# Kernel optimization log

Measured on AMD Instinct MI355X. Metric: run time of the kernel, lower is better.

## Reference

```python
import jax, jax.numpy as jnp
import numpy as np

VOCAB, EMB, RNN, OUT = 32000, 512, 1024, 4


def setup_inputs() -> dict:
    key = jax.random.key(0)
    ks = jax.random.split(key, 8)
    stdv = 1.0 / np.sqrt(RNN)
    u = lambda k, shape, s: jax.random.uniform(k, shape, jnp.float32, -s, s)
    return {
        "x": jax.random.randint(ks[0], (512, 64), 0, VOCAB),
        "emb_table": jax.random.normal(ks[1], (VOCAB, EMB), jnp.float32),
        "w_ih": u(ks[2], (3 * RNN, EMB), stdv),
        "w_hh": u(ks[3], (3 * RNN, RNN), stdv),
        "b_ih": u(ks[4], (3 * RNN,), stdv),
        "b_hh": u(ks[5], (3 * RNN,), stdv),
        "fc_w": u(ks[6], (OUT, RNN), 1.0 / np.sqrt(RNN)),
        "fc_b": u(ks[7], (OUT,), 1.0 / np.sqrt(RNN)),
    }


def reference(x, emb_table, w_ih, w_hh, b_ih, b_hh, fc_w, fc_b):
    # x: [T, B] int indices
    T, B = x.shape
    embedded = emb_table[x]  # [T, B, EMB]
    # precompute input projections for all timesteps at once: [T, B, 3*RNN]
    gi_all = jnp.einsum('tbe,ge->tbg', embedded, w_ih) + b_ih

    def step(h, gi):
        gh = h @ w_hh.T + b_hh  # [B, 3*RNN]
        i_r, i_i, i_n = jnp.split(gi, 3, axis=1)
        h_r, h_i, h_n = jnp.split(gh, 3, axis=1)
        r = jax.nn.sigmoid(i_r + h_r)
        z = jax.nn.sigmoid(i_i + h_i)
        n = jnp.tanh(i_n + r * h_n)
        hy = z * n + (1.0 - z) * h  # note: matches GRUCellExposed (z gates newgate)
        return hy, hy

    h0 = jnp.zeros((B, w_hh.shape[1]), embedded.dtype)
    h_last, _ = jax.lax.scan(step, h0, gi_all)
    out = h_last @ fc_w.T + fc_b  # [B, OUT]
    return out
```

## Files before the change

kernel.cpp:

```cpp
#include <hip/hip_runtime.h>
#include <hip/hip_bf16.h>

typedef __attribute__((ext_vector_type(8))) short  short8;
typedef __attribute__((ext_vector_type(4))) float  f32x4;

#define T_TOTAL 512
#define BATCH   64
#define VOCAB   32000
#define EMB     512
#define RNN     1024
#define G3      3072
#define WROWS   48
#define WPAD    1032
#define RPAD    18
#define NWG     256
#define NGRP    4
#define SMEM_BYTES (WROWS * WPAD * 2 + 4 * WROWS * RPAD * 4)

__device__ __forceinline__ unsigned short f2bf(float f) {
    union { float f; unsigned int u; } v; v.f = f;
    unsigned int r = v.u + 0x7fffu + ((v.u >> 16) & 1u);
    return (unsigned short)(r >> 16);
}
__device__ __forceinline__ float bf2f(unsigned short h) {
    union { unsigned int u; float f; } v; v.u = ((unsigned int)h) << 16;
    return v.f;
}
__device__ __forceinline__ float sigmoidf_(float x) { return 1.f / (1.f + __expf(-x)); }
__device__ __forceinline__ float tanhf_(float x) {
    float ax = fabsf(x);
    float e2 = __expf(-2.f * ax);
    float t  = (1.f - e2) / (1.f + e2);
    return x < 0.f ? -t : t;
}

__device__ __forceinline__ void gbar_arrive(unsigned int* flags, int sidx,
                                            unsigned int ph) {
    __syncthreads();
    if (threadIdx.x == 0)
        __hip_atomic_store(&flags[sidx], ph,
                           __ATOMIC_RELAXED, __HIP_MEMORY_SCOPE_AGENT);
}
__device__ __forceinline__ void gbar_wait(unsigned int* flags, unsigned int ph) {
    if (threadIdx.x < 64) {
        for (;;) {
            unsigned int v = __hip_atomic_load(&flags[threadIdx.x],
                                               __ATOMIC_RELAXED,
                                               __HIP_MEMORY_SCOPE_AGENT);
            if (__all(v >= ph)) break;
            __builtin_amdgcn_s_sleep(1);
        }
    }
    __syncthreads();
}

__global__ void bar_init(unsigned int* bar) {
    for (int i = threadIdx.x; i < NGRP * 256; i += 256) bar[i] = 0;
}

__global__ __launch_bounds__(256) void cvt_bf16_kernel(
    const float* __restrict__ s, unsigned short* __restrict__ d, int n8)
{
    const int i = blockIdx.x * 256 + threadIdx.x;
    if (i >= n8) return;
    const float4 a = ((const float4*)s)[i * 2];
    const float4 b = ((const float4*)s)[i * 2 + 1];
    short8 v;
    v[0] = f2bf(a.x); v[1] = f2bf(a.y); v[2] = f2bf(a.z); v[3] = f2bf(a.w);
    v[4] = f2bf(b.x); v[5] = f2bf(b.y); v[6] = f2bf(b.z); v[7] = f2bf(b.w);
    ((short8*)d)[i] = v;
}

template<bool BF>
__global__ __launch_bounds__(256) void gi_kernel(
    const int* __restrict__ x, const void* __restrict__ embp,
    const void* __restrict__ wihp, const float* __restrict__ b_ih,
    unsigned short* __restrict__ gi, int t0)
{
    __shared__ __align__(16) unsigned short Asm[128 * 40];
    __shared__ __align__(16) unsigned short Bsm[128 * 40];

    const int tid = threadIdx.x;
    const int m0 = blockIdx.x * 128;
    const int n0 = blockIdx.y * 128;

    const int r    = tid >> 1;
    const int half = tid & 1;
    const int xi = x[t0 * BATCH + m0 + r];
    unsigned short* adst = &Asm[r * 40 + half * 16];
    unsigned short* bdst = &Bsm[r * 40 + half * 16];

    const int lane = tid & 63, wv = tid >> 6;
    const int m_off = (wv & 1) * 64, n_off = (wv >> 1) * 64;
    const int lr = lane & 15, lq = lane >> 4;

    f32x4 acc[4][4];
    #pragma unroll
    for (int i = 0; i < 4; ++i)
        #pragma unroll
        for (int j = 0; j < 4; ++j) acc[i][j] = (f32x4){0.f, 0.f, 0.f, 0.f};

    if constexpr (BF) {
        const unsigned short* arow = (const unsigned short*)embp
                                   + (size_t)xi * EMB + half * 16;
        const unsigned short* brow = (const unsigned short*)wihp
                                   + (size_t)(n0 + r) * EMB + half * 16;
        for (int k0 = 0; k0 < EMB; k0 += 32) {
            const short8 av0 = *(const short8*)(arow + k0);
            const short8 av1 = *(const short8*)(arow + k0 + 8);
            const short8 bv0 = *(const short8*)(brow + k0);
            const short8 bv1 = *(const short8*)(brow + k0 + 8);
            __syncthreads();
            *(short8*)(adst)     = av0;
            *(short8*)(adst + 8) = av1;
            *(short8*)(bdst)     = bv0;
            *(short8*)(bdst + 8) = bv1;
            __syncthreads();

            short8 fa[4], fb[4];
            #pragma unroll
            for (int i = 0; i < 4; ++i) {
                fa[i] = *(const short8*)&Asm[(m_off + i * 16 + lr) * 40 + lq * 8];
                fb[i] = *(const short8*)&Bsm[(n_off + i * 16 + lr) * 40 + lq * 8];
            }
            #pragma unroll
            for (int mi = 0; mi < 4; ++mi)
                #pragma unroll
                for (int ni = 0; ni < 4; ++ni)
                    acc[mi][ni] = __builtin_amdgcn_mfma_f32_16x16x32_bf16(
                        fa[mi], fb[ni], acc[mi][ni], 0, 0, 0);
        }
    } else {
        const float* arow = (const float*)embp + (size_t)xi * EMB + half * 16;
        const float* brow = (const float*)wihp + (size_t)(n0 + r) * EMB + half * 16;
        for (int k0 = 0; k0 < EMB; k0 += 32) {
            const float4 a0 = *(const float4*)(arow + k0);
            const float4 a1 = *(const float4*)(arow + k0 + 4);
            const float4 a2 = *(const float4*)(arow + k0 + 8);
            const float4 a3 = *(const float4*)(arow + k0 + 12);
            const float4 b0 = *(const float4*)(brow + k0);
            const float4 b1 = *(const float4*)(brow + k0 + 4);
            const float4 b2 = *(const float4*)(brow + k0 + 8);
            const float4 b3 = *(const float4*)(brow + k0 + 12);
            __syncthreads();
            short8 av0, av1, bv0, bv1;
            av0[0]=f2bf(a0.x); av0[1]=f2bf(a0.y); av0[2]=f2bf(a0.z); av0[3]=f2bf(a0.w);
            av0[4]=f2bf(a1.x); av0[5]=f2bf(a1.y); av0[6]=f2bf(a1.z); av0[7]=f2bf(a1.w);
            av1[0]=f2bf(a2.x); av1[1]=f2bf(a2.y); av1[2]=f2bf(a2.z); av1[3]=f2bf(a2.w);
            av1[4]=f2bf(a3.x); av1[5]=f2bf(a3.y); av1[6]=f2bf(a3.z); av1[7]=f2bf(a3.w);
            bv0[0]=f2bf(b0.x); bv0[1]=f2bf(b0.y); bv0[2]=f2bf(b0.z); bv0[3]=f2bf(b0.w);
            bv0[4]=f2bf(b1.x); bv0[5]=f2bf(b1.y); bv0[6]=f2bf(b1.z); bv0[7]=f2bf(b1.w);
            bv1[0]=f2bf(b2.x); bv1[1]=f2bf(b2.y); bv1[2]=f2bf(b2.z); bv1[3]=f2bf(b2.w);
            bv1[4]=f2bf(b3.x); bv1[5]=f2bf(b3.y); bv1[6]=f2bf(b3.z); bv1[7]=f2bf(b3.w);
            *(short8*)(adst)     = av0;
            *(short8*)(adst + 8) = av1;
            *(short8*)(bdst)     = bv0;
            *(short8*)(bdst + 8) = bv1;
            __syncthreads();

            short8 fa[4], fb[4];
            #pragma unroll
            for (int i = 0; i < 4; ++i) {
                fa[i] = *(const short8*)&Asm[(m_off + i * 16 + lr) * 40 + lq * 8];
                fb[i] = *(const short8*)&Bsm[(n_off + i * 16 + lr) * 40 + lq * 8];
            }
            #pragma unroll
            for (int mi = 0; mi < 4; ++mi)
                #pragma unroll
                for (int ni = 0; ni < 4; ++ni)
                    acc[mi][ni] = __builtin_amdgcn_mfma_f32_16x16x32_bf16(
                        fa[mi], fb[ni], acc[mi][ni], 0, 0, 0);
        }
    }

    float bia[4];
    #pragma unroll
    for (int ni = 0; ni < 4; ++ni) bia[ni] = b_ih[n0 + n_off + ni * 16 + lr];
    #pragma unroll
    for (int mi = 0; mi < 4; ++mi)
        #pragma unroll
        for (int ni = 0; ni < 4; ++ni) {
            const int n = n0 + n_off + ni * 16 + lr;
            #pragma unroll
            for (int q = 0; q < 4; ++q) {
                const int m = m0 + m_off + mi * 16 + lq * 4 + q;
                gi[(size_t)m * G3 + n] = f2bf(acc[mi][ni][q] + bia[ni]);
            }
        }
}

__global__ __launch_bounds__(256, 1) void rec_kernel(
    const unsigned short* __restrict__ gi,
    const float* __restrict__ w_hh, const float* __restrict__ b_hh,
    unsigned short* __restrict__ hb0, unsigned short* __restrict__ hb1,
    float* __restrict__ hf, unsigned int* bar, int t0, int nsteps, int pbase)
{
    extern __shared__ __align__(16) char smem[];
    unsigned short* Wsm = (unsigned short*)smem;
    float (*red)[WROWS][RPAD] = (float (*)[WROWS][RPAD])(smem + WROWS * WPAD * 2);

    const int tid = threadIdx.x;
    const int wg  = blockIdx.x;
    const int grp = wg & 3, sidx = wg >> 2;
    const int b0 = grp * 16, j0 = sidx * 16;
    unsigned int* flags = &bar[grp * 64];

    #pragma unroll 4
    for (int it = 0; it < 48; ++it) {
        const int i   = it * 256 + tid;
        const int row = i >> 8;
        const int c4  = (i & 255) * 4;
        const int gate = row >> 4, uu = row & 15;
        const float4 v = *(const float4*)(w_hh + (size_t)(gate * RNN + j0 + uu) * RNN + c4);
        unsigned short* dst = &Wsm[row * WPAD + c4];
        dst[0] = f2bf(v.x); dst[1] = f2bf(v.y); dst[2] = f2bf(v.z); dst[3] = f2bf(v.w);
    }

    const int u  = tid & 15;
    const int bl = tid >> 4;
    const int j  = j0 + u;
    const int b  = b0 + bl;
    const float bhr = b_hh[j], bhi = b_hh[RNN + j], bhn = b_hh[2 * RNN + j];

    float h_reg;
    if (t0 == 0) {
        h_reg = 0.f;
        if ((u & 1) == 0)
            __hip_atomic_store((unsigned int*)&hb0[b * RNN + j], 0u,
                               __ATOMIC_RELAXED, __HIP_MEMORY_SCOPE_AGENT);
    } else {
        h_reg = hf[b * RNN + j];
    }
    gbar_arrive(flags, sidx, (unsigned)(pbase + 1));

    size_t gb = (size_t)b * G3 + j0 + u;
    float gir = bf2f(gi[gb]);
    float gii = bf2f(gi[gb + RNN]);
    float gin = bf2f(gi[gb + 2 * RNN]);
    gbar_wait(flags, (unsigned)(pbase + 1));

    const int lane = tid & 63, kq = tid >> 6;
    const int lr = lane & 15, lq = lane >> 4;
    const unsigned short* wbase = Wsm + kq * 256 + lq * 8;
    const size_t hoff = ((size_t)(b0 + lr) * RNN + kq * 256 + lq * 8) >> 2;

    for (int t = 0; t < nsteps; ++t) {
        const unsigned short* hrd = (t & 1) ? hb1 : hb0;
        unsigned short*       hwr = (t & 1) ? hb0 : hb1;

        union { unsigned long long q[2]; short8 s8; } hv[8];
        const unsigned long long* hp = (const unsigned long long*)hrd + hoff;
        #pragma unroll
        for (int ks = 0; ks < 8; ++ks) {
            hv[ks].q[0] = __hip_atomic_load(hp + ks * 8,     __ATOMIC_RELAXED,
                                            __HIP_MEMORY_SCOPE_AGENT);
            hv[ks].q[1] = __hip_atomic_load(hp + ks * 8 + 1, __ATOMIC_RELAXED,
                                            __HIP_MEMORY_SCOPE_AGENT);
        }

        f32x4 acc[3];
        acc[0] = (f32x4){0.f, 0.f, 0.f, 0.f};
        acc[1] = (f32x4){0.f, 0.f, 0.f, 0.f};
        acc[2] = (f32x4){0.f, 0.f, 0.f, 0.f};
        #pragma unroll
        for (int ks = 0; ks < 8; ++ks) {
            const int k = ks * 32;
            #pragma unroll
            for (int gt = 0; gt < 3; ++gt) {
                const short8 a = *(const short8*)(wbase + (gt * 16 + lr) * WPAD + k);
                acc[gt] = __builtin_amdgcn_mfma_f32_16x16x32_bf16(a, hv[ks].s8,
                                                                  acc[gt], 0, 0, 0);
            }
        }
        #pragma unroll
        for (int gt = 0; gt < 3; ++gt)
            #pragma unroll
            for (int q = 0; q < 4; ++q)
                red[kq][gt * 16 + lq * 4 + q][lr] = acc[gt][q];
        __syncthreads();

        const float ghr = red[0][u][bl]      + red[1][u][bl]
                        + red[2][u][bl]      + red[3][u][bl];
        const float ghi = red[0][16 + u][bl] + red[1][16 + u][bl]
                        + red[2][16 + u][bl] + red[3][16 + u][bl];
        const float ghn = red[0][32 + u][bl] + red[1][32 + u][bl]
                        + red[2][32 + u][bl] + red[3][32 + u][bl];
        const float rr = sigmoidf_(gir + ghr + bhr);
        const float zz = sigmoidf_(gii + ghi + bhi);
        const float nn = tanhf_(gin + rr * (ghn + bhn));
        h_reg = zz * nn + (1.f - zz) * h_reg;

        unsigned int hvv = (unsigned int)f2bf(h_reg);
        unsigned int ovv = __shfl_xor((int)hvv, 1);
        if ((u & 1) == 0)
            __hip_atomic_store((unsigned int*)&hwr[b * RNN + j],
                               hvv | (ovv << 16), __ATOMIC_RELAXED,
                               __HIP_MEMORY_SCOPE_AGENT);

        gbar_arrive(flags, sidx, (unsigned)(pbase + 2 + t));
        const int tn = (t + 1 < nsteps) ? t + 1 : t;
        gb = ((size_t)tn * BATCH + b) * G3 + j0 + u;
        const float ngr = bf2f(gi[gb]);
        const float ngi = bf2f(gi[gb + RNN]);
        const float ngn = bf2f(gi[gb + 2 * RNN]);
        gbar_wait(flags, (unsigned)(pbase + 2 + t));
        gir = ngr; gii = ngi; gin = ngn;
    }
    hf[b * RNN + j] = h_reg;
}

__global__ __launch_bounds__(256) void out_kernel(
    const float* __restrict__ hf, const float* __restrict__ fc_w,
    const float* __restrict__ fc_b, float* __restrict__ out)
{
    __shared__ float red[256];
    const int bidx = blockIdx.x, tid = threadIdx.x;
    const int o = tid & 3, seg = tid >> 2;
    const float* hp = hf   + (size_t)bidx * RNN + seg * 16;
    const float* wp = fc_w + (size_t)o * RNN + seg * 16;
    float acc = 0.f;
    #pragma unroll
    for (int i = 0; i < 16; ++i) acc += hp[i] * wp[i];
    red[tid] = acc;
    __syncthreads();
    if (tid < 4) {
        float sv = fc_b[tid];
        #pragma unroll 8
        for (int q = 0; q < 64; ++q) sv += red[q * 4 + tid];
        out[bidx * 4 + tid] = sv;
    }
}

extern "C" void kernel_launch(void* const* d_in, const int* in_sizes, int n_in,
                              void* d_out, int out_size, void* d_ws, size_t ws_size,
                              hipStream_t stream)
{
    const int*   x     = (const int*)d_in[0];
    const float* emb   = (const float*)d_in[1];
    const float* w_ih  = (const float*)d_in[2];
    const float* w_hh  = (const float*)d_in[3];
    const float* b_ih  = (const float*)d_in[4];
    const float* b_hh  = (const float*)d_in[5];
    const float* fc_w  = (const float*)d_in[6];
    const float* fc_b  = (const float*)d_in[7];
    float*       out   = (float*)d_out;

    const size_t bar_b   = (size_t)NGRP * 256 * 4;
    const size_t aux     = 2 * (size_t)BATCH * RNN * 2
                         + (size_t)BATCH * RNN * 4 + bar_b;
    const size_t gi_full = (size_t)T_TOTAL * BATCH * G3 * 2;
    const size_t embbf_b = (size_t)VOCAB * EMB * 2;
    const size_t wihbf_b = (size_t)G3 * EMB * 2;
    const bool fused  = ws_size >= gi_full + aux;
    const bool bfpath = ws_size >= gi_full + aux + embbf_b + wihbf_b;
    const int tch  = fused ? 512 : 128;
    const int nchk = T_TOTAL / tch;

    char* ws = (char*)d_ws;
    unsigned short* gi_buf = (unsigned short*)ws;
    size_t off = (size_t)tch * BATCH * G3 * 2;
    unsigned short* hb0 = (unsigned short*)(ws + off); off += (size_t)BATCH * RNN * 2;
    unsigned short* hb1 = (unsigned short*)(ws + off); off += (size_t)BATCH * RNN * 2;
    float*          hf  = (float*)(ws + off);          off += (size_t)BATCH * RNN * 4;
    unsigned int*   bar = (unsigned int*)(ws + off);   off += bar_b;
    unsigned short* embbf = (unsigned short*)(ws + off); off += embbf_b;
    unsigned short* wihbf = (unsigned short*)(ws + off);

    hipFuncSetAttribute((const void*)rec_kernel,
                        hipFuncAttributeMaxDynamicSharedMemorySize, SMEM_BYTES);

    bar_init<<<dim3(1), dim3(256), 0, stream>>>(bar);
    if (bfpath) {
        cvt_bf16_kernel<<<dim3((VOCAB * EMB / 8 + 255) / 256), dim3(256), 0, stream>>>(
            emb, embbf, VOCAB * EMB / 8);
        cvt_bf16_kernel<<<dim3((G3 * EMB / 8 + 255) / 256), dim3(256), 0, stream>>>(
            w_ih, wihbf, G3 * EMB / 8);
    }

    for (int c = 0; c < nchk; ++c) {
        int t0 = c * tch, ns = tch, pb = c * (tch + 1);
        if (bfpath)
            gi_kernel<true><<<dim3(tch * BATCH / 128, 24), dim3(256), 0, stream>>>(
                x, (const void*)embbf, (const void*)wihbf, b_ih, gi_buf, t0);
        else
            gi_kernel<false><<<dim3(tch * BATCH / 128, 24), dim3(256), 0, stream>>>(
                x, (const void*)emb, (const void*)w_ih, b_ih, gi_buf, t0);
        void* args[10];
        args[0] = (void*)&gi_buf; args[1] = (void*)&w_hh; args[2] = (void*)&b_hh;
        args[3] = (void*)&hb0;    args[4] = (void*)&hb1;  args[5] = (void*)&hf;
        args[6] = (void*)&bar;    args[7] = (void*)&t0;   args[8] = (void*)&ns;
        args[9] = (void*)&pb;
        hipLaunchCooperativeKernel((const void*)rec_kernel, dim3(NWG), dim3(256),
                                   args, SMEM_BYTES, stream);
    }
    out_kernel<<<dim3(BATCH), dim3(256), 0, stream>>>(hf, fc_w, fc_b, out);
}
```

Baseline: 2.243 ms.

## Use counter-based grid barrier and keep gathered embeddings resident in gi GEMM

```diff
diff --git a/kernel.cpp b/kernel.cpp
--- a/kernel.cpp
+++ b/kernel.cpp
@@ -15,7 +15,11 @@
 #define RPAD    18
 #define NWG     256
 #define NGRP    4
+#define NLINE   2
 #define SMEM_BYTES (WROWS * WPAD * 2 + 4 * WROWS * RPAD * 4)
+
+#define APAD    520
+#define GI_SMEM (128 * APAD * 2 + 128 * 40 * 2)
 
 __device__ __forceinline__ unsigned short f2bf(float f) {
     union { float f; unsigned int u; } v; v.f = f;
@@ -34,22 +38,18 @@
     return x < 0.f ? -t : t;
 }
 
-__device__ __forceinline__ void gbar_arrive(unsigned int* flags, int sidx,
+__device__ __forceinline__ void gbar_arrive(unsigned int* lines, int lid,
                                             unsigned int ph) {
     __syncthreads();
     if (threadIdx.x == 0)
-        __hip_atomic_store(&flags[sidx], ph,
-                           __ATOMIC_RELAXED, __HIP_MEMORY_SCOPE_AGENT);
-}
-__device__ __forceinline__ void gbar_wait(unsigned int* flags, unsigned int ph) {
-    if (threadIdx.x < 64) {
-        for (;;) {
-            unsigned int v = __hip_atomic_load(&flags[threadIdx.x],
-                                               __ATOMIC_RELAXED,
-                                               __HIP_MEMORY_SCOPE_AGENT);
-            if (__all(v >= ph)) break;
+        __hip_atomic_fetch_add(&lines[lid * 64], 1u,
+                               __ATOMIC_RELAXED, __HIP_MEMORY_SCOPE_AGENT);
+}
+__device__ __forceinline__ void gbar_wait(unsigned int* lines, unsigned int ph) {
+    if (threadIdx.x < NLINE) {
+        while (__hip_atomic_load(&lines[threadIdx.x * 64], __ATOMIC_RELAXED,
+                                 __HIP_MEMORY_SCOPE_AGENT) < ph * 32u)
             __builtin_amdgcn_s_sleep(1);
-        }
     }
     __syncthreads();
 }
@@ -77,50 +77,88 @@
     const void* __restrict__ wihp, const float* __restrict__ b_ih,
     unsigned short* __restrict__ gi, int t0)
 {
-    __shared__ __align__(16) unsigned short Asm[128 * 40];
-    __shared__ __align__(16) unsigned short Bsm[128 * 40];
+    extern __shared__ __align__(16) unsigned short gsm[];
+    unsigned short* Asm = gsm;
+    unsigned short* Bsm = gsm + 128 * APAD;
 
     const int tid = threadIdx.x;
     const int m0 = blockIdx.x * 128;
-    const int n0 = blockIdx.y * 128;
+    const int nseg   = 24 / gridDim.y;
+    const int nstart = blockIdx.y * nseg;
 
     const int r    = tid >> 1;
     const int half = tid & 1;
     const int xi = x[t0 * BATCH + m0 + r];
-    unsigned short* adst = &Asm[r * 40 + half * 16];
-    unsigned short* bdst = &Bsm[r * 40 + half * 16];
+
+    if constexpr (BF) {
+        const unsigned short* arow = (const unsigned short*)embp
+                                   + (size_t)xi * EMB + half * 16;
+        #pragma unroll 4
+        for (int k0 = 0; k0 < EMB; k0 += 32) {
+            const short8 a0 = *(const short8*)(arow + k0);
+            const short8 a1 = *(const short8*)(arow + k0 + 8);
+            *(short8*)&Asm[r * APAD + k0 + half * 16]     = a0;
+            *(short8*)&Asm[r * APAD + k0 + half * 16 + 8] = a1;
+        }
+    } else {
+        const float* arow = (const float*)embp + (size_t)xi * EMB + half * 16;
+        #pragma unroll 4
+        for (int k0 = 0; k0 < EMB; k0 += 32) {
+            const float4 a0 = *(const float4*)(arow + k0);
+            const float4 a1 = *(const float4*)(arow + k0 + 4);
+            const float4 a2 = *(const float4*)(arow + k0 + 8);
+            const float4 a3 = *(const float4*)(arow + k0 + 12);
+            short8 v0, v1;
+            v0[0]=f2bf(a0.x); v0[1]=f2bf(a0.y); v0[2]=f2bf(a0.z); v0[3]=f2bf(a0.w);
+            v0[4]=f2bf(a1.x); v0[5]=f2bf(a1.y); v0[6]=f2bf(a1.z); v0[7]=f2bf(a1.w);
+            v1[0]=f2bf(a2.x); v1[1]=f2bf(a2.y); v1[2]=f2bf(a2.z); v1[3]=f2bf(a2.w);
+            v1[4]=f2bf(a3.x); v1[5]=f2bf(a3.y); v1[6]=f2bf(a3.z); v1[7]=f2bf(a3.w);
+            *(short8*)&Asm[r * APAD + k0 + half * 16]     = v0;
+            *(short8*)&Asm[r * APAD + k0 + half * 16 + 8] = v1;
+        }
+    }
 
     const int lane = tid & 63, wv = tid >> 6;
     const int m_off = (wv & 1) * 64, n_off = (wv >> 1) * 64;
     const int lr = lane & 15, lq = lane >> 4;
 
-    f32x4 acc[4][4];
-    #pragma unroll
-    for (int i = 0; i < 4; ++i)
-        #pragma unroll
-        for (int j = 0; j < 4; ++j) acc[i][j] = (f32x4){0.f, 0.f, 0.f, 0.f};
-
-    if constexpr (BF) {
-        const unsigned short* arow = (const unsigned short*)embp
-                                   + (size_t)xi * EMB + half * 16;
-        const unsigned short* brow = (const unsigned short*)wihp
-                                   + (size_t)(n0 + r) * EMB + half * 16;
+    for (int nt = 0; nt < nseg; ++nt) {
+        const int n0 = (nstart + nt) * 128;
+
+        f32x4 acc[4][4];
+        #pragma unroll
+        for (int i = 0; i < 4; ++i)
+            #pragma unroll
+            for (int j = 0; j < 4; ++j) acc[i][j] = (f32x4){0.f, 0.f, 0.f, 0.f};
+
         for (int k0 = 0; k0 < EMB; k0 += 32) {
-            const short8 av0 = *(const short8*)(arow + k0);
-            const short8 av1 = *(const short8*)(arow + k0 + 8);
-            const short8 bv0 = *(const short8*)(brow + k0);
-            const short8 bv1 = *(const short8*)(brow + k0 + 8);
+            short8 bv0, bv1;
+            if constexpr (BF) {
+                const unsigned short* brow = (const unsigned short*)wihp
+                                           + (size_t)(n0 + r) * EMB + half * 16;
+                bv0 = *(const short8*)(brow + k0);
+                bv1 = *(const short8*)(brow + k0 + 8);
+            } else {
+                const float* brow = (const float*)wihp
+                                  + (size_t)(n0 + r) * EMB + half * 16;
+                const float4 b0 = *(const float4*)(brow + k0);
+                const float4 b1 = *(const float4*)(brow + k0 + 4);
+                const float4 b2 = *(const float4*)(brow + k0 + 8);
+                const float4 b3 = *(const float4*)(brow + k0 + 12);
+                bv0[0]=f2bf(b0.x); bv0[1]=f2bf(b0.y); bv0[2]=f2bf(b0.z); bv0[3]=f2bf(b0.w);
+                bv0[4]=f2bf(b1.x); bv0[5]=f2bf(b1.y); bv0[6]=f2bf(b1.z); bv0[7]=f2bf(b1.w);
+                bv1[0]=f2bf(b2.x); bv1[1]=f2bf(b2.y); bv1[2]=f2bf(b2.z); bv1[3]=f2bf(b2.w);
+                bv1[4]=f2bf(b3.x); bv1[5]=f2bf(b3.y); bv1[6]=f2bf(b3.z); bv1[7]=f2bf(b3.w);
+            }
             __syncthreads();
-            *(short8*)(adst)     = av0;
-            *(short8*)(adst + 8) = av1;
-            *(short8*)(bdst)     = bv0;
-            *(short8*)(bdst + 8) = bv1;
+            *(short8*)&Bsm[r * 40 + half * 16]     = bv0;
+            *(short8*)&Bsm[r * 40 + half * 16 + 8] = bv1;
             __syncthreads();
 
             short8 fa[4], fb[4];
             #pragma unroll
             for (int i = 0; i < 4; ++i) {
-                fa[i] = *(const short8*)&Asm[(m_off + i * 16 + lr) * 40 + lq * 8];
+                fa[i] = *(const short8*)&Asm[(m_off + i * 16 + lr) * APAD + k0 + lq * 8];
                 fb[i] = *(const short8*)&Bsm[(n_off + i * 16 + lr) * 40 + lq * 8];
             }
             #pragma unroll
@@ -130,63 +168,22 @@
                     acc[mi][ni] = __builtin_amdgcn_mfma_f32_16x16x32_bf16(
                         fa[mi], fb[ni], acc[mi][ni], 0, 0, 0);
         }
-    } else {
-        const float* arow = (const float*)embp + (size_t)xi * EMB + half * 16;
-        const float* brow = (const float*)wihp + (size_t)(n0 + r) * EMB + half * 16;
-        for (int k0 = 0; k0 < EMB; k0 += 32) {
-            const float4 a0 = *(const float4*)(arow + k0);
-            const float4 a1 = *(const float4*)(arow + k0 + 4);
-            const float4 a2 = *(const float4*)(arow + k0 + 8);
-            const float4 a3 = *(const float4*)(arow + k0 + 12);
-            const float4 b0 = *(const float4*)(brow + k0);
-            const float4 b1 = *(const float4*)(brow + k0 + 4);
-            const float4 b2 = *(const float4*)(brow + k0 + 8);
-            const float4 b3 = *(const float4*)(brow + k0 + 12);
-            __syncthreads();
-            short8 av0, av1, bv0, bv1;
-            av0[0]=f2bf(a0.x); av0[1]=f2bf(a0.y); av0[2]=f2bf(a0.z); av0[3]=f2bf(a0.w);
-            av0[4]=f2bf(a1.x); av0[5]=f2bf(a1.y); av0[6]=f2bf(a1.z); av0[7]=f2bf(a1.w);
-            av1[0]=f2bf(a2.x); av1[1]=f2bf(a2.y); av1[2]=f2bf(a2.z); av1[3]=f2bf(a2.w);
-            av1[4]=f2bf(a3.x); av1[5]=f2bf(a3.y); av1[6]=f2bf(a3.z); av1[7]=f2bf(a3.w);
-            bv0[0]=f2bf(b0.x); bv0[1]=f2bf(b0.y); bv0[2]=f2bf(b0.z); bv0[3]=f2bf(b0.w);
-            bv0[4]=f2bf(b1.x); bv0[5]=f2bf(b1.y); bv0[6]=f2bf(b1.z); bv0[7]=f2bf(b1.w);
-            bv1[0]=f2bf(b2.x); bv1[1]=f2bf(b2.y); bv1[2]=f2bf(b2.z); bv1[3]=f2bf(b2.w);
-            bv1[4]=f2bf(b3.x); bv1[5]=f2bf(b3.y); bv1[6]=f2bf(b3.z); bv1[7]=f2bf(b3.w);
-            *(short8*)(adst)     = av0;
-            *(short8*)(adst + 8) = av1;
-            *(short8*)(bdst)     = bv0;
-            *(short8*)(bdst + 8) = bv1;
-            __syncthreads();
-
-            short8 fa[4], fb[4];
-            #pragma unroll
-            for (int i = 0; i < 4; ++i) {
-                fa[i] = *(const short8*)&Asm[(m_off + i * 16 + lr) * 40 + lq * 8];
-                fb[i] = *(const short8*)&Bsm[(n_off + i * 16 + lr) * 40 + lq * 8];
+
+        float bia[4];
+        #pragma unroll
+        for (int ni = 0; ni < 4; ++ni) bia[ni] = b_ih[n0 + n_off + ni * 16 + lr];
+        #pragma unroll
+        for (int mi = 0; mi < 4; ++mi)
+            #pragma unroll
+            for (int ni = 0; ni < 4; ++ni) {
+                const int n = n0 + n_off + ni * 16 + lr;
+                #pragma unroll
+                for (int q = 0; q < 4; ++q) {
+                    const int m = m0 + m_off + mi * 16 + lq * 4 + q;
+                    gi[(size_t)m * G3 + n] = f2bf(acc[mi][ni][q] + bia[ni]);
+                }
             }
-            #pragma unroll
-            for (int mi = 0; mi < 4; ++mi)
-                #pragma unroll
-                for (int ni = 0; ni < 4; ++ni)
-                    acc[mi][ni] = __builtin_amdgcn_mfma_f32_16x16x32_bf16(
-                        fa[mi], fb[ni], acc[mi][ni], 0, 0, 0);
-        }
-    }
-
-    float bia[4];
-    #pragma unroll
-    for (int ni = 0; ni < 4; ++ni) bia[ni] = b_ih[n0 + n_off + ni * 16 + lr];
-    #pragma unroll
-    for (int mi = 0; mi < 4; ++mi)
-        #pragma unroll
-        for (int ni = 0; ni < 4; ++ni) {
-            const int n = n0 + n_off + ni * 16 + lr;
-            #pragma unroll
-            for (int q = 0; q < 4; ++q) {
-                const int m = m0 + m_off + mi * 16 + lq * 4 + q;
-                gi[(size_t)m * G3 + n] = f2bf(acc[mi][ni][q] + bia[ni]);
-            }
-        }
+    }
 }
 
 __global__ __launch_bounds__(256, 1) void rec_kernel(
@@ -203,7 +200,8 @@
     const int wg  = blockIdx.x;
     const int grp = wg & 3, sidx = wg >> 2;
     const int b0 = grp * 16, j0 = sidx * 16;
-    unsigned int* flags = &bar[grp * 64];
+    unsigned int* lines = &bar[grp * 256];
+    const int lid = sidx & (NLINE - 1);
 
     #pragma unroll 4
     for (int it = 0; it < 48; ++it) {
@@ -231,13 +229,13 @@
     } else {
         h_reg = hf[b * RNN + j];
     }
-    gbar_arrive(flags, sidx, (unsigned)(pbase + 1));
+    gbar_arrive(lines, lid, (unsigned)(pbase + 1));
 
     size_t gb = (size_t)b * G3 + j0 + u;
     float gir = bf2f(gi[gb]);
     float gii = bf2f(gi[gb + RNN]);
     float gin = bf2f(gi[gb + 2 * RNN]);
-    gbar_wait(flags, (unsigned)(pbase + 1));
+    gbar_wait(lines, (unsigned)(pbase + 1));
 
     const int lane = tid & 63, kq = tid >> 6;
     const int lr = lane & 15, lq = lane >> 4;
@@ -297,13 +295,13 @@
                                hvv | (ovv << 16), __ATOMIC_RELAXED,
                                __HIP_MEMORY_SCOPE_AGENT);
 
-        gbar_arrive(flags, sidx, (unsigned)(pbase + 2 + t));
+        gbar_arrive(lines, lid, (unsigned)(pbase + 2 + t));
         const int tn = (t + 1 < nsteps) ? t + 1 : t;
         gb = ((size_t)tn * BATCH + b) * G3 + j0 + u;
         const float ngr = bf2f(gi[gb]);
         const float ngi = bf2f(gi[gb + RNN]);
         const float ngn = bf2f(gi[gb + 2 * RNN]);
-        gbar_wait(flags, (unsigned)(pbase + 2 + t));
+        gbar_wait(lines, (unsigned)(pbase + 2 + t));
         gir = ngr; gii = ngi; gin = ngn;
     }
     hf[b * RNN + j] = h_reg;
@@ -368,6 +366,10 @@
 
     hipFuncSetAttribute((const void*)rec_kernel,
                         hipFuncAttributeMaxDynamicSharedMemorySize, SMEM_BYTES);
+    hipFuncSetAttribute((const void*)gi_kernel<true>,
+                        hipFuncAttributeMaxDynamicSharedMemorySize, GI_SMEM);
+    hipFuncSetAttribute((const void*)gi_kernel<false>,
+                        hipFuncAttributeMaxDynamicSharedMemorySize, GI_SMEM);
 
     bar_init<<<dim3(1), dim3(256), 0, stream>>>(bar);
     if (bfpath) {
@@ -379,11 +381,12 @@
 
     for (int c = 0; c < nchk; ++c) {
         int t0 = c * tch, ns = tch, pb = c * (tch + 1);
+        const dim3 gig = fused ? dim3(256, 1) : dim3(64, 4);
         if (bfpath)
-            gi_kernel<true><<<dim3(tch * BATCH / 128, 24), dim3(256), 0, stream>>>(
+            gi_kernel<true><<<gig, dim3(256), GI_SMEM, stream>>>(
                 x, (const void*)embbf, (const void*)wihbf, b_ih, gi_buf, t0);
         else
-            gi_kernel<false><<<dim3(tch * BATCH / 128, 24), dim3(256), 0, stream>>>(
+            gi_kernel<false><<<gig, dim3(256), GI_SMEM, stream>>>(
                 x, (const void*)emb, (const void*)w_ih, b_ih, gi_buf, t0);
         void* args[10];
         args[0] = (void*)&gi_buf; args[1] = (void*)&w_hh; args[2] = (void*)&b_hh;
```

Measured after the change: 2.099 ms. 6.4% less time.
